# Optimization experiments

Hardware: AMD Instinct MI355X
Metric: run time of the kernel (lower is better)

## Reference

```python
import jax, jax.numpy as jnp
import numpy as np

HEAD_DIM = 128


def block_causal_mask(cu_seqlens, seq_len, dtype):
    # positions -> which packed document each token belongs to
    positions = jnp.arange(seq_len)
    seq_ids = jnp.searchsorted(cu_seqlens, positions, side='right') - 1
    same_seq = seq_ids[:, None] == seq_ids[None, :]
    causal = positions[None, :] <= positions[:, None]  # key_pos <= query_pos
    neg_inf = jnp.asarray(float('-inf'), dtype)
    return jnp.where(same_seq & causal, jnp.asarray(0.0, dtype), neg_inf)


def setup_inputs() -> dict:
    key = jax.random.key(0)
    kq, kk, kv = jax.random.split(key, 3)
    B, H, S, D = 1, 8, 4096, HEAD_DIM
    q = jax.random.normal(kq, (B, H, S, D), dtype=jnp.float32)
    k = jax.random.normal(kk, (B, H, S, D), dtype=jnp.float32)
    v = jax.random.normal(kv, (B, H, S, D), dtype=jnp.float32)
    # 4 packed documents of length 1024 each; cu_seqlens[-1] == seq_len
    cu_seqlens = jnp.array([0, 1024, 2048, 3072, 4096], dtype=jnp.int32)
    return {"q": q, "k": k, "v": v, "cu_seqlens": cu_seqlens, "max_seqlen": 1024}


def reference(q, k, v, cu_seqlens, max_seqlen):
    seq_len = q.shape[2]
    scale = 1.0 / jnp.sqrt(jnp.asarray(q.shape[-1], q.dtype))
    mask = block_causal_mask(cu_seqlens, seq_len, q.dtype)  # [S, S]
    # scores: [B, H, Sq, Sk]
    scores = jnp.einsum('bhqd,bhkd->bhqk', q, k) * scale + mask
    probs = jax.nn.softmax(scores, axis=-1)
    return jnp.einsum('bhqk,bhkd->bhqd', probs, v)
```

## Files before the change

kernel.cpp:

```cpp
#include <hip/hip_runtime.h>
#include <hip/hip_bf16.h>


#define HD 128
#define BR 64
#define BC 64
#define KSTR 136
#define VSTR 33
#define PSTR 72

typedef __attribute__((ext_vector_type(8))) short short8;
typedef __attribute__((ext_vector_type(4))) short short4v;
typedef __attribute__((ext_vector_type(4))) float floatx4;

__device__ inline unsigned short bfbits(float f) {
    __hip_bfloat16 b = __float2bfloat16(f);
    return *reinterpret_cast<unsigned short*>(&b);
}
__device__ inline short bfs(float f) {
    __hip_bfloat16 b = __float2bfloat16(f);
    return *reinterpret_cast<short*>(&b);
}

union F4 { float4 v; float f[4]; };

__global__ __launch_bounds__(256, 2) void fa_fwd(
    const float* __restrict__ Q,
    const float* __restrict__ K,
    const float* __restrict__ V,
    const int* __restrict__ cu_seqlens, int n_cu,
    float* __restrict__ O,
    int S)
{
    __shared__ alignas(16) __hip_bfloat16 sK[2][BC * KSTR];
    __shared__ alignas(16) unsigned int   sVT[2][HD * VSTR];
    __shared__ alignas(16) __hip_bfloat16 sP[4][16 * PSTR];

    const int tid  = threadIdx.x;
    const int wave = tid >> 6;
    const int lane = tid & 63;
    const int quad = lane >> 4;
    const int l16  = lane & 15;

    const int dblk = tid & 31;
    const int trow = tid >> 5;

    const int nqb = S / BR;
    const int h   = blockIdx.x & 7;
    const int qb  = nqb - 1 - (int)(blockIdx.x >> 3);
    const int q0  = qb * BR;
    const int qw  = q0 + wave * 16;

    const size_t hoff = (size_t)h * S * HD;
    const float* Qh = Q + hoff;
    const float* Kh = K + hoff;
    const float* Vh = V + hoff;
    float*       Oh = O + hoff;

    int doc_start[4];
    #pragma unroll
    for (int r = 0; r < 4; ++r) {
        const int q = qw + quad * 4 + r;
        int dsr = 0;
        for (int i = 0; i < n_cu; ++i) {
            int c = cu_seqlens[i];
            if (c <= q) dsr = c;
        }
        doc_start[r] = dsr;
    }
    int blk_ds = 0;
    for (int i = 0; i < n_cu; ++i) {
        int c = cu_seqlens[i];
        if (c <= q0) blk_ds = c;
    }
    const int k_begin = blk_ds & ~(BC - 1);
    const int ntiles  = (q0 + BR - 1 - k_begin) / BC + 1;

    short8 aq[4];
    {
        const float* qp = Qh + (size_t)(qw + l16) * HD + quad * 8;
        #pragma unroll
        for (int ks = 0; ks < 4; ++ks) {
            float4 a0 = *(const float4*)(qp + ks * 32);
            float4 a1 = *(const float4*)(qp + ks * 32 + 4);
            short8 a;
            a[0] = bfs(a0.x); a[1] = bfs(a0.y); a[2] = bfs(a0.z); a[3] = bfs(a0.w);
            a[4] = bfs(a1.x); a[5] = bfs(a1.y); a[6] = bfs(a1.z); a[7] = bfs(a1.w);
            aq[ks] = a;
        }
    }

    floatx4 oacc[8];
    #pragma unroll
    for (int dt = 0; dt < 8; ++dt) oacc[dt] = (floatx4){0.f, 0.f, 0.f, 0.f};
    float m_r[4], l_r[4];
    #pragma unroll
    for (int r = 0; r < 4; ++r) { m_r[r] = -1e30f; l_r[r] = 0.f; }

    const float sl = 0.08838834764831845f * 1.4426950408889634f;

    F4 kf[8], vf[2][4];

    auto issue_loads = [&](int kt) {
        const float* kb = Kh + (size_t)kt * HD + 4 * dblk;
        #pragma unroll
        for (int p = 0; p < 8; ++p)
            kf[p].v = *(const float4*)(kb + (size_t)(trow + 8 * p) * HD);
        const float* vb = Vh + (size_t)kt * HD + 4 * dblk;
        #pragma unroll
        for (int p = 0; p < 2; ++p) {
            const int kk = 4 * trow + 32 * p;
            #pragma unroll
            for (int j = 0; j < 4; ++j)
                vf[p][j].v = *(const float4*)(vb + (size_t)(kk + j) * HD);
        }
    };

    auto write_tiles = [&](int buf) {
        #pragma unroll
        for (int p = 0; p < 8; ++p) {
            short4v hk;
            hk[0] = bfs(kf[p].f[0]); hk[1] = bfs(kf[p].f[1]);
            hk[2] = bfs(kf[p].f[2]); hk[3] = bfs(kf[p].f[3]);
            *(short4v*)(&sK[buf][(trow + 8 * p) * KSTR + 4 * dblk]) = hk;
        }
        #pragma unroll
        for (int p = 0; p < 2; ++p) {
            const int kp0 = (4 * trow + 32 * p) >> 1;
            #pragma unroll
            for (int i = 0; i < 4; ++i) {
                unsigned d0 = ((unsigned)bfbits(vf[p][1].f[i]) << 16) | bfbits(vf[p][0].f[i]);
                unsigned d1 = ((unsigned)bfbits(vf[p][3].f[i]) << 16) | bfbits(vf[p][2].f[i]);
                unsigned* dst = &sVT[buf][(4 * dblk + i) * VSTR + kp0];
                dst[0] = d0;
                dst[1] = d1;
            }
        }
    };

    issue_loads(k_begin);

    __hip_bfloat16* pbuf = &sP[wave][0];

    for (int it = 0; it < ntiles; ++it) {
        const int kt  = k_begin + it * BC;
        const int buf = it & 1;

        write_tiles(buf);
        __syncthreads();

        if (it + 1 < ntiles) issue_loads(kt + BC);

        floatx4 sc[4];
        #pragma unroll
        for (int ct = 0; ct < 4; ++ct) {
            floatx4 c = (floatx4){0.f, 0.f, 0.f, 0.f};
            #pragma unroll
            for (int ks = 0; ks < 4; ++ks) {
                short8 b = *(const short8*)(&sK[buf][(ct * 16 + l16) * KSTR + ks * 32 + quad * 8]);
                c = __builtin_amdgcn_mfma_f32_16x16x32_bf16(aq[ks], b, c, 0, 0, 0);
            }
            sc[ct] = c;
        }

        #pragma unroll
        for (int ct = 0; ct < 4; ++ct) {
            const int key = kt + ct * 16 + l16;
            #pragma unroll
            for (int r = 0; r < 4; ++r) {
                const int q = qw + quad * 4 + r;
                const bool valid = (key <= q) && (key >= doc_start[r]);
                float s = sc[ct][r] * sl;
                sc[ct][r] = valid ? s : -1e30f;
            }
        }

        float mx[4];
        #pragma unroll
        for (int r = 0; r < 4; ++r)
            mx[r] = fmaxf(fmaxf(sc[0][r], sc[1][r]), fmaxf(sc[2][r], sc[3][r]));
        #pragma unroll
        for (int off = 1; off < 16; off <<= 1) {
            #pragma unroll
            for (int r = 0; r < 4; ++r)
                mx[r] = fmaxf(mx[r], __shfl_xor(mx[r], off, 64));
        }
        float al[4];
        #pragma unroll
        for (int r = 0; r < 4; ++r) {
            const float mnew = fmaxf(m_r[r], mx[r]);
            al[r] = exp2f(m_r[r] - mnew);
            m_r[r] = mnew;
        }
        float ps[4];
        #pragma unroll
        for (int r = 0; r < 4; ++r) {
            float s0 = exp2f(sc[0][r] - m_r[r]);
            float s1 = exp2f(sc[1][r] - m_r[r]);
            float s2 = exp2f(sc[2][r] - m_r[r]);
            float s3 = exp2f(sc[3][r] - m_r[r]);
            sc[0][r] = s0; sc[1][r] = s1; sc[2][r] = s2; sc[3][r] = s3;
            ps[r] = (s0 + s1) + (s2 + s3);
        }
        #pragma unroll
        for (int off = 1; off < 16; off <<= 1) {
            #pragma unroll
            for (int r = 0; r < 4; ++r)
                ps[r] += __shfl_xor(ps[r], off, 64);
        }
        #pragma unroll
        for (int r = 0; r < 4; ++r)
            l_r[r] = l_r[r] * al[r] + ps[r];
        #pragma unroll
        for (int dt = 0; dt < 8; ++dt) {
            #pragma unroll
            for (int r = 0; r < 4; ++r)
                oacc[dt][r] *= al[r];
        }

        #pragma unroll
        for (int ct = 0; ct < 4; ++ct)
            #pragma unroll
            for (int r = 0; r < 4; ++r)
                pbuf[(quad * 4 + r) * PSTR + ct * 16 + l16] = __float2bfloat16(sc[ct][r]);

        #pragma unroll
        for (int ks = 0; ks < 2; ++ks) {
            short8 ap = *(const short8*)(&pbuf[l16 * PSTR + ks * 32 + quad * 8]);
            #pragma unroll
            for (int dt = 0; dt < 8; ++dt) {
                const unsigned* vp = &sVT[buf][(dt * 16 + l16) * VSTR + ks * 16 + quad * 4];
                union { unsigned u[4]; short8 s; } cv;
                cv.u[0] = vp[0]; cv.u[1] = vp[1]; cv.u[2] = vp[2]; cv.u[3] = vp[3];
                oacc[dt] = __builtin_amdgcn_mfma_f32_16x16x32_bf16(ap, cv.s, oacc[dt], 0, 0, 0);
            }
        }
    }

    #pragma unroll
    for (int r = 0; r < 4; ++r) {
        const float inv = 1.0f / l_r[r];
        float* op = Oh + (size_t)(qw + quad * 4 + r) * HD;
        #pragma unroll
        for (int dt = 0; dt < 8; ++dt)
            op[dt * 16 + l16] = oacc[dt][r] * inv;
    }
}

extern "C" void kernel_launch(void* const* d_in, const int* in_sizes, int n_in,
                              void* d_out, int out_size, void* d_ws, size_t ws_size,
                              hipStream_t stream) {
    const float* q = (const float*)d_in[0];
    const float* k = (const float*)d_in[1];
    const float* v = (const float*)d_in[2];
    const int* cu = (const int*)d_in[3];
    const int n_cu = in_sizes[3];
    const int H = 8;
    const int S = in_sizes[0] / (H * HD);
    float* out = (float*)d_out;

    dim3 grid(H * (S / BR));
    dim3 block(256);
    fa_fwd<<<grid, block, 0, stream>>>(q, k, v, cu, n_cu, out, S);
}
```

Baseline: 145.7 us.

## Skip fully masked causal subtiles, defer row-sum reduction, restructure V transpose

Skips QK and PV MFMAs for 16-key subtiles that lie entirely above the causal diagonal for each wave. Moves the per-tile cross-lane reduction of the softmax row sum out of the loop into a single reduction at the end, which is valid because the per-lane partial sums are rescaled by the same alpha. Also changes V loading to scalar coalesced per-column loads with a simpler transpose write into shared memory, and narrows the P stride, reading P with two 8-byte loads. The scalar V loads issue many more load instructions, and the narrower P stride may change bank-conflict behaviour.

```diff
diff --git a/kernel.cpp b/kernel.cpp
--- a/kernel.cpp
+++ b/kernel.cpp
@@ -7,7 +7,7 @@
 #define BC 64
 #define KSTR 136
 #define VSTR 33
-#define PSTR 72
+#define PSTR 68
 
 typedef __attribute__((ext_vector_type(8))) short short8;
 typedef __attribute__((ext_vector_type(4))) short short4v;
@@ -44,6 +44,8 @@
 
     const int dblk = tid & 31;
     const int trow = tid >> 5;
+    const int vd    = tid & 127;
+    const int vhalf = tid >> 7;
 
     const int nqb = S / BR;
     const int h   = blockIdx.x & 7;
@@ -99,21 +101,18 @@
 
     const float sl = 0.08838834764831845f * 1.4426950408889634f;
 
-    F4 kf[8], vf[2][4];
+    F4 kf[8];
+    float vf[32];
 
     auto issue_loads = [&](int kt) {
         const float* kb = Kh + (size_t)kt * HD + 4 * dblk;
         #pragma unroll
         for (int p = 0; p < 8; ++p)
             kf[p].v = *(const float4*)(kb + (size_t)(trow + 8 * p) * HD);
-        const float* vb = Vh + (size_t)kt * HD + 4 * dblk;
-        #pragma unroll
-        for (int p = 0; p < 2; ++p) {
-            const int kk = 4 * trow + 32 * p;
-            #pragma unroll
-            for (int j = 0; j < 4; ++j)
-                vf[p][j].v = *(const float4*)(vb + (size_t)(kk + j) * HD);
-        }
+        const float* vb = Vh + (size_t)(kt + vhalf * 32) * HD + vd;
+        #pragma unroll
+        for (int kk = 0; kk < 32; ++kk)
+            vf[kk] = vb[(size_t)kk * HD];
     };
 
     auto write_tiles = [&](int buf) {
@@ -124,18 +123,10 @@
             hk[2] = bfs(kf[p].f[2]); hk[3] = bfs(kf[p].f[3]);
             *(short4v*)(&sK[buf][(trow + 8 * p) * KSTR + 4 * dblk]) = hk;
         }
-        #pragma unroll
-        for (int p = 0; p < 2; ++p) {
-            const int kp0 = (4 * trow + 32 * p) >> 1;
-            #pragma unroll
-            for (int i = 0; i < 4; ++i) {
-                unsigned d0 = ((unsigned)bfbits(vf[p][1].f[i]) << 16) | bfbits(vf[p][0].f[i]);
-                unsigned d1 = ((unsigned)bfbits(vf[p][3].f[i]) << 16) | bfbits(vf[p][2].f[i]);
-                unsigned* dst = &sVT[buf][(4 * dblk + i) * VSTR + kp0];
-                dst[0] = d0;
-                dst[1] = d1;
-            }
-        }
+        unsigned* dst = &sVT[buf][vd * VSTR + vhalf * 16];
+        #pragma unroll
+        for (int kp = 0; kp < 16; ++kp)
+            dst[kp] = ((unsigned)bfbits(vf[2 * kp + 1]) << 16) | bfbits(vf[2 * kp]);
     };
 
     issue_loads(k_begin);
@@ -154,24 +145,24 @@
         floatx4 sc[4];
         #pragma unroll
         for (int ct = 0; ct < 4; ++ct) {
-            floatx4 c = (floatx4){0.f, 0.f, 0.f, 0.f};
-            #pragma unroll
-            for (int ks = 0; ks < 4; ++ks) {
-                short8 b = *(const short8*)(&sK[buf][(ct * 16 + l16) * KSTR + ks * 32 + quad * 8]);
-                c = __builtin_amdgcn_mfma_f32_16x16x32_bf16(aq[ks], b, c, 0, 0, 0);
-            }
-            sc[ct] = c;
-        }
-
-        #pragma unroll
-        for (int ct = 0; ct < 4; ++ct) {
-            const int key = kt + ct * 16 + l16;
-            #pragma unroll
-            for (int r = 0; r < 4; ++r) {
-                const int q = qw + quad * 4 + r;
-                const bool valid = (key <= q) && (key >= doc_start[r]);
-                float s = sc[ct][r] * sl;
-                sc[ct][r] = valid ? s : -1e30f;
+            if (kt + ct * 16 <= qw + 15) {
+                floatx4 c = (floatx4){0.f, 0.f, 0.f, 0.f};
+                #pragma unroll
+                for (int ks = 0; ks < 4; ++ks) {
+                    short8 b = *(const short8*)(&sK[buf][(ct * 16 + l16) * KSTR + ks * 32 + quad * 8]);
+                    c = __builtin_amdgcn_mfma_f32_16x16x32_bf16(aq[ks], b, c, 0, 0, 0);
+                }
+                const int key = kt + ct * 16 + l16;
+                #pragma unroll
+                for (int r = 0; r < 4; ++r) {
+                    const int q = qw + quad * 4 + r;
+                    const bool valid = (key <= q) && (key >= doc_start[r]);
+                    float s = c[r] * sl;
+                    c[r] = valid ? s : -1e30f;
+                }
+                sc[ct] = c;
+            } else {
+                sc[ct] = (floatx4){-1e30f, -1e30f, -1e30f, -1e30f};
             }
         }
 
@@ -192,7 +183,6 @@
             al[r] = exp2f(m_r[r] - mnew);
             m_r[r] = mnew;
         }
-        float ps[4];
         #pragma unroll
         for (int r = 0; r < 4; ++r) {
             float s0 = exp2f(sc[0][r] - m_r[r]);
@@ -200,17 +190,8 @@
             float s2 = exp2f(sc[2][r] - m_r[r]);
             float s3 = exp2f(sc[3][r] - m_r[r]);
             sc[0][r] = s0; sc[1][r] = s1; sc[2][r] = s2; sc[3][r] = s3;
-            ps[r] = (s0 + s1) + (s2 + s3);
-        }
-        #pragma unroll
-        for (int off = 1; off < 16; off <<= 1) {
-            #pragma unroll
-            for (int r = 0; r < 4; ++r)
-                ps[r] += __shfl_xor(ps[r], off, 64);
-        }
-        #pragma unroll
-        for (int r = 0; r < 4; ++r)
-            l_r[r] = l_r[r] * al[r] + ps[r];
+            l_r[r] = l_r[r] * al[r] + ((s0 + s1) + (s2 + s3));
+        }
         #pragma unroll
         for (int dt = 0; dt < 8; ++dt) {
             #pragma unroll
@@ -226,17 +207,27 @@
 
         #pragma unroll
         for (int ks = 0; ks < 2; ++ks) {
-            short8 ap = *(const short8*)(&pbuf[l16 * PSTR + ks * 32 + quad * 8]);
-            #pragma unroll
-            for (int dt = 0; dt < 8; ++dt) {
-                const unsigned* vp = &sVT[buf][(dt * 16 + l16) * VSTR + ks * 16 + quad * 4];
-                union { unsigned u[4]; short8 s; } cv;
-                cv.u[0] = vp[0]; cv.u[1] = vp[1]; cv.u[2] = vp[2]; cv.u[3] = vp[3];
-                oacc[dt] = __builtin_amdgcn_mfma_f32_16x16x32_bf16(ap, cv.s, oacc[dt], 0, 0, 0);
+            if (kt + ks * 32 <= qw + 15) {
+                short4v lo = *(const short4v*)(&pbuf[l16 * PSTR + ks * 32 + quad * 8]);
+                short4v hi = *(const short4v*)(&pbuf[l16 * PSTR + ks * 32 + quad * 8 + 4]);
+                short8 ap = __builtin_shufflevector(lo, hi, 0, 1, 2, 3, 4, 5, 6, 7);
+                #pragma unroll
+                for (int dt = 0; dt < 8; ++dt) {
+                    const unsigned* vp = &sVT[buf][(dt * 16 + l16) * VSTR + ks * 16 + quad * 4];
+                    union { unsigned u[4]; short8 s; } cv;
+                    cv.u[0] = vp[0]; cv.u[1] = vp[1]; cv.u[2] = vp[2]; cv.u[3] = vp[3];
+                    oacc[dt] = __builtin_amdgcn_mfma_f32_16x16x32_bf16(ap, cv.s, oacc[dt], 0, 0, 0);
+                }
             }
         }
     }
 
+    #pragma unroll
+    for (int off = 1; off < 16; off <<= 1) {
+        #pragma unroll
+        for (int r = 0; r < 4; ++r)
+            l_r[r] += __shfl_xor(l_r[r], off, 64);
+    }
     #pragma unroll
     for (int r = 0; r < 4; ++r) {
         const float inv = 1.0f / l_r[r];
```

Result: faster. 141.6 us (-2.8%).
